# Optimization experiments

Measured on AMD Instinct MI355X. Metric: run time of the kernel, lower is better.

## Reference

```python
import jax, jax.numpy as jnp
import numpy as np

B = 262144   # batch_size
DX = 4       # dim_x (state vector 4)
DIMS = [DX, 32, 32, 64, 64, DX]  # fc1, fc_add1, fc2, fc_add2, fc3


def _glorot(key, fan_in, fan_out):
    std = (2.0 / (fan_in + fan_out)) ** 0.5
    return jax.random.normal(key, (fan_in, fan_out), dtype=jnp.float32) * std


def setup_inputs() -> dict:
    key = jax.random.key(0)
    ks = jax.random.split(key, 6)
    inp = {}
    for i in range(5):
        inp[f"W{i+1}"] = _glorot(ks[i], DIMS[i], DIMS[i + 1])
        inp[f"b{i+1}"] = jnp.zeros((DIMS[i + 1],), dtype=jnp.float32)
    inp["last_state"] = jax.random.normal(ks[5], (B, 1, DX), dtype=jnp.float32)
    inp["training"] = 1
    return inp


def _mlp(x, W1, b1, W2, b2, W3, b3, W4, b4, W5, b5):
    # fc1 -> fc_add1 -> fc2 -> fc_add2 -> fc3 (last layer linear)
    h = jax.nn.relu(x @ W1 + b1)
    h = jax.nn.relu(h @ W2 + b2)
    h = jax.nn.relu(h @ W3 + b3)
    h = jax.nn.relu(h @ W4 + b4)
    return h @ W5 + b5


def reference(last_state, W1, b1, W2, b2, W3, b3, W4, b4, W5, b5, training):
    # new_state = last_state + MLP(last_state), shape [B, 1, DX]
    new_state = last_state + _mlp(last_state, W1, b1, W2, b2, W3, b3, W4, b4, W5, b5)

    # batch Jacobian F = d new_state / d last_state, reshaped to [B, DX, DX]
    xs = last_state[:, 0, :]  # [B, DX]

    def f(v):  # per-sample residual update, v: [DX]
        return v + _mlp(v, W1, b1, W2, b2, W3, b3, W4, b4, W5, b5)

    F = jax.vmap(jax.jacfwd(f))(xs)  # [B, DX, DX]; jacfwd is cheap: only DX=4 tangents
    return new_state, F
```

## Files before the change

### kernel.cpp

```cpp
#include <hip/hip_runtime.h>

typedef __attribute__((ext_vector_type(8))) short short8;
typedef __attribute__((ext_vector_type(4))) float f32x4;
typedef __attribute__((ext_vector_type(4))) unsigned uint4v;

#define NWAVES 2
#define BLOCK (64 * NWAVES)
#define TB 8192
#define FWDU 34
#define FWDB (FWDU * 64 * 4)
#define WBYTES (FWDB + 6 * 64 * 4)

__device__ __forceinline__ unsigned short f2bf(float f) {
    unsigned u = __builtin_bit_cast(unsigned, f);
    u += 0x7FFFu + ((u >> 16) & 1u);
    return (unsigned short)(u >> 16);
}

__device__ __forceinline__ int taddr(int row, int slot) {
    return row * 128 + (((slot ^ (row & 7)) << 4));
}

__device__ __forceinline__ short8 loadB(const float* __restrict__ W, int Nout, int Kin,
                                        int kbase, int col) {
    short8 r;
#pragma unroll
    for (int i = 0; i < 8; ++i) {
        int k = kbase + i;
        float v = (k < Kin && col < Nout) ? W[k * Nout + col] : 0.0f;
        r[i] = (short)f2bf(v);
    }
    return r;
}

template<int WORD0, int WSHIFT>
__device__ __forceinline__ void epi_store(unsigned char* wb, const unsigned* mkT,
                                          f32x4 c, int mt, int nt, int lane)
{
    const int col = lane & 15, G = lane >> 4;
    const int unit = nt * 16 + col;
    const int word = WORD0 + (WSHIFT ? (unit >> 5) : 0);
    const int bit  = unit & 31;
    const int R0 = mt * 16 + G * 4;
    const uint4v mw = *(const uint4v*)(mkT + word * 64 + R0);
    const int slot = unit >> 3;
    const int off = (unit & 7) * 2;
#pragma unroll
    for (int i = 0; i < 4; ++i) {
        const int R = R0 + i;
        const float v = ((mw[i] >> bit) & 1u) ? c[i] : 0.0f;
        *(unsigned short*)(wb + R * 128 + (((slot ^ (R & 7)) << 4) | off)) = f2bf(v);
    }
}

template<int KT, int NT, int WORD0, int WSHIFT>
__device__ __forceinline__ void tan_layer_mfma(unsigned char* wb, const unsigned* mkT,
                                               const short8* Bf, int lane)
{
    const int G = lane >> 4;
    const int r15 = lane & 15;
#pragma unroll
    for (int mt = 0; mt < 4; ++mt) {
        const int R = mt * 16 + r15;
        short8 a[KT];
#pragma unroll
        for (int kt = 0; kt < KT; ++kt)
            a[kt] = *(const short8*)(wb + taddr(R, 4 * kt + G));
#pragma unroll
        for (int nt = 0; nt < NT; ++nt) {
            f32x4 c = {0.f, 0.f, 0.f, 0.f};
#pragma unroll
            for (int kt = 0; kt < KT; ++kt)
                c = __builtin_amdgcn_mfma_f32_16x16x32_bf16(a[kt], Bf[kt * NT + nt], c, 0, 0, 0);
            epi_store<WORD0, WSHIFT>(wb, mkT, c, mt, nt, lane);
        }
    }
}

__device__ __forceinline__ void tan_final(unsigned char* wb, const short8* B5,
                                          int lane, int r,
                                          float* __restrict__ out_F, int sbase)
{
    const int G = lane >> 4, col = lane & 15;
    const int r15 = lane & 15;
#pragma unroll
    for (int mt = 0; mt < 4; ++mt) {
        const int R = mt * 16 + r15;
        short8 a0 = *(const short8*)(wb + taddr(R, G));
        short8 a1 = *(const short8*)(wb + taddr(R, 4 + G));
        f32x4 c = {0.f, 0.f, 0.f, 0.f};
        c = __builtin_amdgcn_mfma_f32_16x16x32_bf16(a0, B5[0], c, 0, 0, 0);
        c = __builtin_amdgcn_mfma_f32_16x16x32_bf16(a1, B5[1], c, 0, 0, 0);
        if (col < 4) {
            const int R0 = mt * 16 + G * 4;
#pragma unroll
            for (int i = 0; i < 4; ++i) {
                const float v = c[i] + ((col == r) ? 1.0f : 0.0f);
                out_F[(size_t)(sbase + R0 + i) * 16 + col * 4 + r] = v;
            }
        }
    }
}

__global__ __launch_bounds__(BLOCK)
void mlp_jac_kernel(
    const float* __restrict__ W1, const float* __restrict__ b1,
    const float* __restrict__ W2, const float* __restrict__ b2,
    const float* __restrict__ W3, const float* __restrict__ b3,
    const float* __restrict__ W4, const float* __restrict__ b4,
    const float* __restrict__ W5, const float* __restrict__ b5,
    const float* __restrict__ xin,
    float* __restrict__ out_state, float* __restrict__ out_F, int Btot)
{
    __shared__ __align__(16) unsigned char smem[NWAVES][WBYTES];
    const int tid = threadIdx.x;
    const int wid = tid >> 6;
    const int lane = tid & 63;
    const int sbase = blockIdx.x * BLOCK + wid * 64;
    if (sbase >= Btot) return;

    unsigned char* wb = smem[wid];
    float* fbuf = (float*)wb;
    unsigned* mkT = (unsigned*)(wb + FWDB);

    const int s_my = sbase + lane;
    const float4 xv = *reinterpret_cast<const float4*>(xin + 4 * s_my);
    const float xa[4] = {xv.x, xv.y, xv.z, xv.w};

    unsigned m1, m2;
    unsigned long long m3, m4;
    {
        float acc[32];
#pragma unroll
        for (int j = 0; j < 32; ++j) {
            float a = b1[j];
#pragma unroll
            for (int k = 0; k < 4; ++k) a = fmaf(xa[k], W1[k * 32 + j], a);
            acc[j] = a;
        }
        unsigned m = 0;
#pragma unroll
        for (int j = 0; j < 32; ++j) {
            const bool p = acc[j] > 0.0f;
            m |= ((unsigned)(p ? 1 : 0)) << j;
            fbuf[j * 64 + lane] = p ? acc[j] : 0.0f;
        }
        m1 = m;
    }
    {
        float acc[32];
#pragma unroll
        for (int j = 0; j < 32; ++j) acc[j] = b2[j];
#pragma unroll 2
        for (int k = 0; k < 32; ++k) {
            const float cv = fbuf[k * 64 + lane];
#pragma unroll
            for (int j = 0; j < 32; ++j) acc[j] = fmaf(cv, W2[k * 32 + j], acc[j]);
        }
        unsigned m = 0;
#pragma unroll
        for (int j = 0; j < 32; ++j) {
            const bool p = acc[j] > 0.0f;
            m |= ((unsigned)(p ? 1 : 0)) << j;
            fbuf[j * 64 + lane] = p ? acc[j] : 0.0f;
        }
        m2 = m;
    }
    float h3r[64 - FWDU];
    {
        float acc[64];
#pragma unroll
        for (int j = 0; j < 64; ++j) acc[j] = b3[j];
#pragma unroll 2
        for (int k = 0; k < 32; ++k) {
            const float cv = fbuf[k * 64 + lane];
#pragma unroll
            for (int j = 0; j < 64; ++j) acc[j] = fmaf(cv, W3[k * 64 + j], acc[j]);
        }
        unsigned long long m = 0ULL;
#pragma unroll
        for (int j = 0; j < 64; ++j) {
            const bool p = acc[j] > 0.0f;
            m |= ((unsigned long long)(p ? 1 : 0)) << j;
            const float hv = p ? acc[j] : 0.0f;
            if (j < FWDU) fbuf[j * 64 + lane] = hv;
            else          h3r[j - FWDU] = hv;
        }
        m3 = m;
    }
    {
        float acc[64];
#pragma unroll
        for (int j = 0; j < 64; ++j) acc[j] = b4[j];
#pragma unroll 2
        for (int k = 0; k < FWDU; ++k) {
            const float cv = fbuf[k * 64 + lane];
#pragma unroll
            for (int j = 0; j < 64; ++j) acc[j] = fmaf(cv, W4[k * 64 + j], acc[j]);
        }
#pragma unroll
        for (int t = 0; t < 64 - FWDU; ++t) {
            const float cv = h3r[t];
#pragma unroll
            for (int j = 0; j < 64; ++j) acc[j] = fmaf(cv, W4[(FWDU + t) * 64 + j], acc[j]);
        }
        unsigned long long m = 0ULL;
        float y[4] = {b5[0], b5[1], b5[2], b5[3]};
#pragma unroll
        for (int j = 0; j < 64; ++j) {
            const bool p = acc[j] > 0.0f;
            m |= ((unsigned long long)(p ? 1 : 0)) << j;
            const float hv = p ? acc[j] : 0.0f;
#pragma unroll
            for (int i = 0; i < 4; ++i) y[i] = fmaf(hv, W5[j * 4 + i], y[i]);
        }
        m4 = m;
        float4 o;
        o.x = xa[0] + y[0]; o.y = xa[1] + y[1];
        o.z = xa[2] + y[2]; o.w = xa[3] + y[3];
        *reinterpret_cast<float4*>(out_state + 4 * s_my) = o;
    }
    mkT[0 * 64 + lane] = m1;
    mkT[1 * 64 + lane] = m2;
    mkT[2 * 64 + lane] = (unsigned)(m3 & 0xffffffffULL);
    mkT[3 * 64 + lane] = (unsigned)(m3 >> 32);
    mkT[4 * 64 + lane] = (unsigned)(m4 & 0xffffffffULL);
    mkT[5 * 64 + lane] = (unsigned)(m4 >> 32);

    __builtin_amdgcn_sched_barrier(0);

    const int col = lane & 15, G = lane >> 4;
    short8 B2f[2], B3f[4], B4f[8], B5f[2];
#pragma unroll
    for (int nt = 0; nt < 2; ++nt) B2f[nt] = loadB(W2, 32, 32, 8 * G, 16 * nt + col);
#pragma unroll
    for (int nt = 0; nt < 4; ++nt) B3f[nt] = loadB(W3, 64, 32, 8 * G, 16 * nt + col);
#pragma unroll
    for (int kt = 0; kt < 2; ++kt)
#pragma unroll
        for (int nt = 0; nt < 4; ++nt)
            B4f[kt * 4 + nt] = loadB(W4, 64, 64, 32 * kt + 8 * G, 16 * nt + col);
#pragma unroll
    for (int kt = 0; kt < 2; ++kt) B5f[kt] = loadB(W5, 4, 64, 32 * kt + 8 * G, col);

    for (int r = 0; r < 4; ++r) {
#pragma unroll
        for (int sl = 0; sl < 4; ++sl) {
            short8 v;
#pragma unroll
            for (int e = 0; e < 8; ++e) {
                const int u = sl * 8 + e;
                v[e] = ((m1 >> u) & 1u) ? (short)f2bf(W1[r * 32 + u]) : (short)0;
            }
            *(short8*)(wb + taddr(lane, sl)) = v;
        }
        tan_layer_mfma<1, 2, 1, 0>(wb, mkT, B2f, lane);
        tan_layer_mfma<1, 4, 2, 1>(wb, mkT, B3f, lane);
        tan_layer_mfma<2, 4, 4, 1>(wb, mkT, B4f, lane);
        tan_final(wb, B5f, lane, r, out_F, sbase);
    }
}

extern "C" void kernel_launch(void* const* d_in, const int* in_sizes, int n_in,
                              void* d_out, int out_size, void* d_ws, size_t ws_size,
                              hipStream_t stream)
{
    const float* W1 = (const float*)d_in[0];
    const float* b1 = (const float*)d_in[1];
    const float* W2 = (const float*)d_in[2];
    const float* b2 = (const float*)d_in[3];
    const float* W3 = (const float*)d_in[4];
    const float* b3 = (const float*)d_in[5];
    const float* W4 = (const float*)d_in[6];
    const float* b4 = (const float*)d_in[7];
    const float* W5 = (const float*)d_in[8];
    const float* b5 = (const float*)d_in[9];
    const float* xin = (const float*)d_in[10];

    const int Btot = in_sizes[10] / 4;
    float* out_state = (float*)d_out;
    float* out_F = out_state + (size_t)Btot * 4;

    const int grid = (Btot + BLOCK - 1) / BLOCK;
    mlp_jac_kernel<<<grid, BLOCK, 0, stream>>>(
        W1, b1, W2, b2, W3, b3, W4, b4, W5, b5, xin, out_state, out_F, Btot);
}
```

Baseline: 117.2 us.

## Transpose tangent MFMA so weights are A operand and store packed bf16 rows

Swaps the MFMA operand roles in the tangent (Jacobian) layers so that weight fragments act as the A matrix and the per-sample tangent rows act as B. Each lane's accumulator then holds four consecutive output units of one sample. The masked results can be packed with v_cvt_pk_bf16_f32 and written as one 8-byte LDS store, replacing four scattered 2-byte stores. The ReLU mask words are moved to a per-sample layout so each lane reads its own words once per tile, and the final layer writes F rows directly. The aim is less LDS store traffic and less per-element epilogue work, at the cost of a different mask and LDS access pattern that could raise bank conflicts.

Measured after the change: 108.4 us. 1.08x faster.

```diff
diff --git a/kernel.cpp b/kernel.cpp
--- a/kernel.cpp
+++ b/kernel.cpp
@@ -2,7 +2,7 @@
 
 typedef __attribute__((ext_vector_type(8))) short short8;
 typedef __attribute__((ext_vector_type(4))) float f32x4;
-typedef __attribute__((ext_vector_type(4))) unsigned uint4v;
+typedef __attribute__((ext_vector_type(2))) unsigned uint2v;
 
 #define NWAVES 2
 #define BLOCK (64 * NWAVES)
@@ -33,71 +33,59 @@
     return r;
 }
 
-template<int WORD0, int WSHIFT>
-__device__ __forceinline__ void epi_store(unsigned char* wb, const unsigned* mkT,
-                                          f32x4 c, int mt, int nt, int lane)
-{
-    const int col = lane & 15, G = lane >> 4;
-    const int unit = nt * 16 + col;
-    const int word = WORD0 + (WSHIFT ? (unit >> 5) : 0);
-    const int bit  = unit & 31;
-    const int R0 = mt * 16 + G * 4;
-    const uint4v mw = *(const uint4v*)(mkT + word * 64 + R0);
-    const int slot = unit >> 3;
-    const int off = (unit & 7) * 2;
-#pragma unroll
-    for (int i = 0; i < 4; ++i) {
-        const int R = R0 + i;
-        const float v = ((mw[i] >> bit) & 1u) ? c[i] : 0.0f;
-        *(unsigned short*)(wb + R * 128 + (((slot ^ (R & 7)) << 4) | off)) = f2bf(v);
-    }
-}
-
-template<int KT, int NT, int WORD0, int WSHIFT>
-__device__ __forceinline__ void tan_layer_mfma(unsigned char* wb, const unsigned* mkT,
-                                               const short8* Bf, int lane)
-{
-    const int G = lane >> 4;
-    const int r15 = lane & 15;
-#pragma unroll
-    for (int mt = 0; mt < 4; ++mt) {
-        const int R = mt * 16 + r15;
-        short8 a[KT];
+template<int MT, int KT, int W0, int NW>
+__device__ __forceinline__ void tan_layer_T(unsigned char* wb, const unsigned* mkS,
+                                            const short8* Wf, int lane)
+{
+    const int G = lane >> 4, sl = lane & 15;
+#pragma unroll
+    for (int nt = 0; nt < 4; ++nt) {
+        const int s = nt * 16 + sl;
+        short8 bt[KT];
 #pragma unroll
         for (int kt = 0; kt < KT; ++kt)
-            a[kt] = *(const short8*)(wb + taddr(R, 4 * kt + G));
-#pragma unroll
-        for (int nt = 0; nt < NT; ++nt) {
+            bt[kt] = *(const short8*)(wb + taddr(s, 4 * kt + G));
+        unsigned mwords[NW];
+#pragma unroll
+        for (int w = 0; w < NW; ++w) mwords[w] = mkS[s * 6 + W0 + w];
+#pragma unroll
+        for (int mt = 0; mt < MT; ++mt) {
             f32x4 c = {0.f, 0.f, 0.f, 0.f};
 #pragma unroll
             for (int kt = 0; kt < KT; ++kt)
-                c = __builtin_amdgcn_mfma_f32_16x16x32_bf16(a[kt], Bf[kt * NT + nt], c, 0, 0, 0);
-            epi_store<WORD0, WSHIFT>(wb, mkT, c, mt, nt, lane);
-        }
-    }
-}
-
-__device__ __forceinline__ void tan_final(unsigned char* wb, const short8* B5,
-                                          int lane, int r,
-                                          float* __restrict__ out_F, int sbase)
-{
-    const int G = lane >> 4, col = lane & 15;
-    const int r15 = lane & 15;
-#pragma unroll
-    for (int mt = 0; mt < 4; ++mt) {
-        const int R = mt * 16 + r15;
-        short8 a0 = *(const short8*)(wb + taddr(R, G));
-        short8 a1 = *(const short8*)(wb + taddr(R, 4 + G));
+                c = __builtin_amdgcn_mfma_f32_16x16x32_bf16(Wf[kt * MT + mt], bt[kt], c, 0, 0, 0);
+            const unsigned mw = mwords[(mt * 16) >> 5] >> ((mt & 1) * 16 + G * 4);
+            const float v0 = (mw & 1u) ? c[0] : 0.0f;
+            const float v1 = (mw & 2u) ? c[1] : 0.0f;
+            const float v2 = (mw & 4u) ? c[2] : 0.0f;
+            const float v3 = (mw & 8u) ? c[3] : 0.0f;
+            unsigned lo, hi;
+            asm("v_cvt_pk_bf16_f32 %0, %1, %2" : "=v"(lo) : "v"(v0), "v"(v1));
+            asm("v_cvt_pk_bf16_f32 %0, %1, %2" : "=v"(hi) : "v"(v2), "v"(v3));
+            const int slot = 2 * mt + (G >> 1);
+            uint2v pk; pk[0] = lo; pk[1] = hi;
+            *(uint2v*)(wb + s * 128 + ((slot ^ (s & 7)) << 4) + 8 * (G & 1)) = pk;
+        }
+    }
+}
+
+__device__ __forceinline__ void tan_final_T(unsigned char* wb, const short8* B5,
+                                            int lane, int r,
+                                            float* __restrict__ out_F, int sbase)
+{
+    const int G = lane >> 4, sl = lane & 15;
+#pragma unroll
+    for (int nt = 0; nt < 4; ++nt) {
+        const int s = nt * 16 + sl;
+        short8 b0 = *(const short8*)(wb + taddr(s, G));
+        short8 b1 = *(const short8*)(wb + taddr(s, 4 + G));
         f32x4 c = {0.f, 0.f, 0.f, 0.f};
-        c = __builtin_amdgcn_mfma_f32_16x16x32_bf16(a0, B5[0], c, 0, 0, 0);
-        c = __builtin_amdgcn_mfma_f32_16x16x32_bf16(a1, B5[1], c, 0, 0, 0);
-        if (col < 4) {
-            const int R0 = mt * 16 + G * 4;
-#pragma unroll
-            for (int i = 0; i < 4; ++i) {
-                const float v = c[i] + ((col == r) ? 1.0f : 0.0f);
-                out_F[(size_t)(sbase + R0 + i) * 16 + col * 4 + r] = v;
-            }
+        c = __builtin_amdgcn_mfma_f32_16x16x32_bf16(B5[0], b0, c, 0, 0, 0);
+        c = __builtin_amdgcn_mfma_f32_16x16x32_bf16(B5[1], b1, c, 0, 0, 0);
+        if (G == 0) {
+#pragma unroll
+            for (int i = 0; i < 4; ++i)
+                out_F[(size_t)(sbase + s) * 16 + i * 4 + r] = c[i] + ((i == r) ? 1.0f : 0.0f);
         }
     }
 }
@@ -121,7 +109,7 @@
 
     unsigned char* wb = smem[wid];
     float* fbuf = (float*)wb;
-    unsigned* mkT = (unsigned*)(wb + FWDB);
+    unsigned* mkS = (unsigned*)(wb + FWDB);
 
     const int s_my = sbase + lane;
     const float4 xv = *reinterpret_cast<const float4*>(xin + 4 * s_my);
@@ -220,28 +208,28 @@
         o.z = xa[2] + y[2]; o.w = xa[3] + y[3];
         *reinterpret_cast<float4*>(out_state + 4 * s_my) = o;
     }
-    mkT[0 * 64 + lane] = m1;
-    mkT[1 * 64 + lane] = m2;
-    mkT[2 * 64 + lane] = (unsigned)(m3 & 0xffffffffULL);
-    mkT[3 * 64 + lane] = (unsigned)(m3 >> 32);
-    mkT[4 * 64 + lane] = (unsigned)(m4 & 0xffffffffULL);
-    mkT[5 * 64 + lane] = (unsigned)(m4 >> 32);
+    mkS[lane * 6 + 0] = m1;
+    mkS[lane * 6 + 1] = m2;
+    mkS[lane * 6 + 2] = (unsigned)(m3 & 0xffffffffULL);
+    mkS[lane * 6 + 3] = (unsigned)(m3 >> 32);
+    mkS[lane * 6 + 4] = (unsigned)(m4 & 0xffffffffULL);
+    mkS[lane * 6 + 5] = (unsigned)(m4 >> 32);
 
     __builtin_amdgcn_sched_barrier(0);
 
     const int col = lane & 15, G = lane >> 4;
-    short8 B2f[2], B3f[4], B4f[8], B5f[2];
-#pragma unroll
-    for (int nt = 0; nt < 2; ++nt) B2f[nt] = loadB(W2, 32, 32, 8 * G, 16 * nt + col);
-#pragma unroll
-    for (int nt = 0; nt < 4; ++nt) B3f[nt] = loadB(W3, 64, 32, 8 * G, 16 * nt + col);
+    short8 W2f[2], W3f[4], W4f[8], W5f[2];
+#pragma unroll
+    for (int mt = 0; mt < 2; ++mt) W2f[mt] = loadB(W2, 32, 32, 8 * G, 16 * mt + col);
+#pragma unroll
+    for (int mt = 0; mt < 4; ++mt) W3f[mt] = loadB(W3, 64, 32, 8 * G, 16 * mt + col);
 #pragma unroll
     for (int kt = 0; kt < 2; ++kt)
 #pragma unroll
-        for (int nt = 0; nt < 4; ++nt)
-            B4f[kt * 4 + nt] = loadB(W4, 64, 64, 32 * kt + 8 * G, 16 * nt + col);
-#pragma unroll
-    for (int kt = 0; kt < 2; ++kt) B5f[kt] = loadB(W5, 4, 64, 32 * kt + 8 * G, col);
+        for (int mt = 0; mt < 4; ++mt)
+            W4f[kt * 4 + mt] = loadB(W4, 64, 64, 32 * kt + 8 * G, 16 * mt + col);
+#pragma unroll
+    for (int kt = 0; kt < 2; ++kt) W5f[kt] = loadB(W5, 4, 64, 32 * kt + 8 * G, col);
 
     for (int r = 0; r < 4; ++r) {
 #pragma unroll
@@ -254,10 +242,10 @@
             }
             *(short8*)(wb + taddr(lane, sl)) = v;
         }
-        tan_layer_mfma<1, 2, 1, 0>(wb, mkT, B2f, lane);
-        tan_layer_mfma<1, 4, 2, 1>(wb, mkT, B3f, lane);
-        tan_layer_mfma<2, 4, 4, 1>(wb, mkT, B4f, lane);
-        tan_final(wb, B5f, lane, r, out_F, sbase);
+        tan_layer_T<2, 1, 1, 1>(wb, mkS, W2f, lane);
+        tan_layer_T<4, 1, 2, 2>(wb, mkS, W3f, lane);
+        tan_layer_T<4, 2, 4, 2>(wb, mkS, W4f, lane);
+        tan_final_T(wb, W5f, lane, r, out_F, sbase);
     }
 }
 
```
